# Optimization experiments

Hardware: AMD Instinct MI355X
Metric: run time of the kernel (lower is better)

Reference implementation:

```python
import jax, jax.numpy as jnp
import numpy as np
import math

B, S, IN_DIM, D, L, W = 16, 2048, 32, 512, 6, 3
FF = 4 * D
EPS = 1e-5
MAX_LEN = 5000


def _make_pe(d_model, max_len=MAX_LEN):
    position = np.arange(max_len, dtype=np.float32)[:, None]
    div_term = np.exp(np.arange(0, d_model, 2, dtype=np.float32) * (-math.log(10000.0) / d_model))
    pe = np.zeros((max_len, d_model), np.float32)
    pe[:, 0::2] = np.sin(position * div_term)
    pe[:, 1::2] = np.cos(position * div_term)
    # register_buffer pe: [max_len, 1, d_model] (seq-first layout)
    return jnp.asarray(pe[:, None, :])


def setup_inputs() -> dict:
    key = jax.random.key(0)
    ks = jax.random.split(key, 16)
    s = 0.02
    inp = {
        "src": jax.random.normal(ks[0], (B, S, IN_DIM), jnp.float32),
        "pe": _make_pe(D),
        "enc_w": jax.random.uniform(ks[1], (D, IN_DIM), jnp.float32, -0.1, 0.1),
        "enc_b": jnp.zeros((D,), jnp.float32),
        "l1_w": jax.random.normal(ks[2], (L, FF, D), jnp.float32) * s,
        "l1_b": jnp.zeros((L, FF), jnp.float32),
        "l2_w": jax.random.normal(ks[3], (L, D, FF), jnp.float32) * s,
        "l2_b": jnp.zeros((L, D), jnp.float32),
        "n1_g": jnp.ones((L, D), jnp.float32),
        "n1_b": jnp.zeros((L, D), jnp.float32),
        "n2_g": jnp.ones((L, D), jnp.float32),
        "n2_b": jnp.zeros((L, D), jnp.float32),
        "dec_w": jax.random.uniform(ks[4], (1, D), jnp.float32, -0.1, 0.1),
        "dec_b": jnp.zeros((1,), jnp.float32),
    }
    return inp


def _layernorm(x, g, b):
    mu = jnp.mean(x, axis=-1, keepdims=True)
    var = jnp.var(x, axis=-1, keepdims=True)
    return (x - mu) * jax.lax.rsqrt(var + EPS) * g + b


def _sparse_attention(q, k, v, window):
    # banded local attention: query i attends to keys j with |i-j| <= window
    Bq, Sq, Dq = q.shape
    scale = 1.0 / math.sqrt(Dq)
    offs = jnp.arange(2 * window + 1) - window          # [K]
    idx = jnp.arange(Sq)[:, None] + offs[None, :]        # [S, K]
    valid = (idx >= 0) & (idx < Sq)
    idxc = jnp.clip(idx, 0, Sq - 1)
    kw = k[:, idxc]                                      # [B, S, K, D]
    vw = v[:, idxc]                                      # [B, S, K, D]
    scores = jnp.einsum('bsd,bskd->bsk', q, kw) * scale  # [B, S, K]
    scores = jnp.where(valid[None, :, :], scores, -1e9)
    attn = jax.nn.softmax(scores, axis=-1)
    return jnp.einsum('bsk,bskd->bsd', attn, vw)


def reference(src, pe, enc_w, enc_b, l1_w, l1_b, l2_w, l2_b,
              n1_g, n1_b, n2_g, n2_b, dec_w, dec_b):
    x = src @ enc_w.T + enc_b
    x = x * math.sqrt(D)
    # faithful to original: pe[:x.size(0)] -> [B,1,D] broadcast over seq
    x = x + pe[: x.shape[0]]
    for i in range(L):
        a = _sparse_attention(x, x, x, W)
        x = _layernorm(x + a, n1_g[i], n1_b[i])
        h = jax.nn.relu(x @ l1_w[i].T + l1_b[i])
        f = h @ l2_w[i].T + l2_b[i]
        x = _layernorm(x + f, n2_g[i], n2_b[i])
    out = x[:, -1, :] @ dec_w.T + dec_b  # [B, 1]
    return out
```

## Files before the change

kernel.cpp:

```cpp
#include <hip/hip_runtime.h>
#include <hip/hip_bf16.h>
#include <math.h>

constexpr int Bb  = 16;
constexpr int Ss  = 2048;
constexpr int INd = 32;
constexpr int Dd  = 512;
constexpr int FFf = 2048;
constexpr int Ll  = 6;
constexpr int BS  = Bb * Ss;
constexpr float EPSf = 1e-5f;

typedef __attribute__((ext_vector_type(8))) short short8;
typedef __attribute__((ext_vector_type(4))) float f32x4;

__device__ __forceinline__ ushort f2bf(float f) {
    uint u = __float_as_uint(f);
    uint r = (u + 0x7fffu + ((u >> 16) & 1u)) >> 16;
    return (ushort)r;
}

__global__ __launch_bounds__(256)
void convert_bf16(const float* __restrict__ in, ushort* __restrict__ out, int n4) {
    int i = blockIdx.x * blockDim.x + threadIdx.x;
    int stride = gridDim.x * blockDim.x;
    for (; i < n4; i += stride) {
        float4 v = ((const float4*)in)[i];
        ushort4 o;
        o.x = f2bf(v.x); o.y = f2bf(v.y); o.z = f2bf(v.z); o.w = f2bf(v.w);
        ((ushort4*)out)[i] = o;
    }
}

__global__ __launch_bounds__(256)
void encode_kernel(const float* __restrict__ src, const float* __restrict__ pe,
                   const float* __restrict__ ew, const float* __restrict__ eb,
                   float* __restrict__ y) {
    __shared__ float s_src[8][32];
    const int tid = threadIdx.x;
    const int d0  = 2 * tid;
    float w0[32], w1[32];
    #pragma unroll
    for (int k = 0; k < 32; k += 4) {
        float4 a = *(const float4*)(ew + (size_t)d0 * INd + k);
        float4 b = *(const float4*)(ew + (size_t)(d0 + 1) * INd + k);
        w0[k] = a.x; w0[k+1] = a.y; w0[k+2] = a.z; w0[k+3] = a.w;
        w1[k] = b.x; w1[k+1] = b.y; w1[k+2] = b.z; w1[k+3] = b.w;
    }
    const float e0 = eb[d0], e1 = eb[d0 + 1];
    const float sqrtD = 22.62741699796952f;

    for (int t0 = 0; t0 < BS / 2048; t0 += 8) {
        __syncthreads();
        {
            const int j = tid >> 5, e = tid & 31;
            const int tok = (int)blockIdx.x + (t0 + j) * 2048;
            s_src[j][e] = src[(size_t)tok * INd + e];
        }
        __syncthreads();
        #pragma unroll
        for (int j = 0; j < 8; ++j) {
            const int tok = (int)blockIdx.x + (t0 + j) * 2048;
            const int b   = tok >> 11;
            float a0 = 0.f, a1 = 0.f;
            #pragma unroll
            for (int k = 0; k < 32; ++k) {
                const float sv = s_src[j][k];
                a0 = fmaf(sv, w0[k], a0);
                a1 = fmaf(sv, w1[k], a1);
            }
            const float2 pv = *(const float2*)(pe + (size_t)b * Dd + d0);
            float2 o;
            o.x = (a0 + e0) * sqrtD + pv.x;
            o.y = (a1 + e1) * sqrtD + pv.y;
            *(float2*)(y + (size_t)tok * Dd + d0) = o;
        }
    }
}

__global__ __launch_bounds__(256)
void attn_ln_kernel(const float* __restrict__ x, float* __restrict__ y,
                    ushort* __restrict__ ybf,
                    const float* __restrict__ g, const float* __restrict__ bb) {
    const int wv   = threadIdx.x >> 6;
    const int lane = threadIdx.x & 63;
    const int wid  = blockIdx.x * 4 + wv;
    const int b    = wid >> 11;
    const int s    = wid & (Ss - 1);
    const float* base = x + (size_t)b * Ss * Dd;

    float rows[7][8];
    #pragma unroll
    for (int o = 0; o < 7; ++o) {
        int sp = s + o - 3;
        int sc = sp < 0 ? 0 : (sp > Ss - 1 ? Ss - 1 : sp);
        const float* r = base + (size_t)sc * Dd;
        float4 v0 = *(const float4*)(r + lane * 4);
        float4 v1 = *(const float4*)(r + 256 + lane * 4);
        rows[o][0] = v0.x; rows[o][1] = v0.y; rows[o][2] = v0.z; rows[o][3] = v0.w;
        rows[o][4] = v1.x; rows[o][5] = v1.y; rows[o][6] = v1.z; rows[o][7] = v1.w;
    }

    const float scale = 0.04419417382415922f;
    float score[7];
    #pragma unroll
    for (int o = 0; o < 7; ++o) {
        float p = 0.f;
        #pragma unroll
        for (int j = 0; j < 8; ++j) p = fmaf(rows[3][j], rows[o][j], p);
        #pragma unroll
        for (int m = 1; m < 64; m <<= 1) p += __shfl_xor(p, m, 64);
        int sp = s + o - 3;
        score[o] = (sp >= 0 && sp < Ss) ? p * scale : -1e9f;
    }
    float mx = score[0];
    #pragma unroll
    for (int o = 1; o < 7; ++o) mx = fmaxf(mx, score[o]);
    float w[7], wsum = 0.f;
    #pragma unroll
    for (int o = 0; o < 7; ++o) { w[o] = __expf(score[o] - mx); wsum += w[o]; }
    const float inv = 1.f / wsum;
    #pragma unroll
    for (int o = 0; o < 7; ++o) w[o] *= inv;

    float r2[8];
    #pragma unroll
    for (int j = 0; j < 8; ++j) {
        float acc = rows[3][j];
        #pragma unroll
        for (int o = 0; o < 7; ++o) acc = fmaf(w[o], rows[o][j], acc);
        r2[j] = acc;
    }

    float sm = 0.f, sq = 0.f;
    #pragma unroll
    for (int j = 0; j < 8; ++j) { sm += r2[j]; sq = fmaf(r2[j], r2[j], sq); }
    #pragma unroll
    for (int m = 1; m < 64; m <<= 1) {
        sm += __shfl_xor(sm, m, 64);
        sq += __shfl_xor(sq, m, 64);
    }
    const float mu   = sm * (1.f / Dd);
    const float var  = sq * (1.f / Dd) - mu * mu;
    const float rstd = rsqrtf(var + EPSf);

    const size_t ob = (size_t)wid * Dd;
    float4 g0 = *(const float4*)(g  + lane * 4);
    float4 b0 = *(const float4*)(bb + lane * 4);
    float4 g1 = *(const float4*)(g  + 256 + lane * 4);
    float4 b1 = *(const float4*)(bb + 256 + lane * 4);
    float4 o0, o1;
    o0.x = (r2[0] - mu) * rstd * g0.x + b0.x;
    o0.y = (r2[1] - mu) * rstd * g0.y + b0.y;
    o0.z = (r2[2] - mu) * rstd * g0.z + b0.z;
    o0.w = (r2[3] - mu) * rstd * g0.w + b0.w;
    o1.x = (r2[4] - mu) * rstd * g1.x + b1.x;
    o1.y = (r2[5] - mu) * rstd * g1.y + b1.y;
    o1.z = (r2[6] - mu) * rstd * g1.z + b1.z;
    o1.w = (r2[7] - mu) * rstd * g1.w + b1.w;
    *(float4*)(y + ob + lane * 4)       = o0;
    *(float4*)(y + ob + 256 + lane * 4) = o1;

    ushort4 q0, q1;
    q0.x = f2bf(o0.x); q0.y = f2bf(o0.y); q0.z = f2bf(o0.z); q0.w = f2bf(o0.w);
    q1.x = f2bf(o1.x); q1.y = f2bf(o1.y); q1.z = f2bf(o1.z); q1.w = f2bf(o1.w);
    *(ushort4*)(ybf + ob + lane * 4)       = q0;
    *(ushort4*)(ybf + ob + 256 + lane * 4) = q1;
}

__global__ __launch_bounds__(256)
void add_ln_kernel(const float* __restrict__ xres, float* __restrict__ f,
                   const float* __restrict__ g, const float* __restrict__ bb) {
    const int wv   = threadIdx.x >> 6;
    const int lane = threadIdx.x & 63;
    const int wid  = blockIdx.x * 4 + wv;
    const size_t ob = (size_t)wid * Dd;

    float4 a0 = *(const float4*)(xres + ob + lane * 4);
    float4 f0 = *(const float4*)(f    + ob + lane * 4);
    float4 a1 = *(const float4*)(xres + ob + 256 + lane * 4);
    float4 f1 = *(const float4*)(f    + ob + 256 + lane * 4);
    float r2[8];
    r2[0] = a0.x + f0.x; r2[1] = a0.y + f0.y; r2[2] = a0.z + f0.z; r2[3] = a0.w + f0.w;
    r2[4] = a1.x + f1.x; r2[5] = a1.y + f1.y; r2[6] = a1.z + f1.z; r2[7] = a1.w + f1.w;

    float sm = 0.f, sq = 0.f;
    #pragma unroll
    for (int j = 0; j < 8; ++j) { sm += r2[j]; sq = fmaf(r2[j], r2[j], sq); }
    #pragma unroll
    for (int m = 1; m < 64; m <<= 1) {
        sm += __shfl_xor(sm, m, 64);
        sq += __shfl_xor(sq, m, 64);
    }
    const float mu   = sm * (1.f / Dd);
    const float var  = sq * (1.f / Dd) - mu * mu;
    const float rstd = rsqrtf(var + EPSf);

    float4 g0 = *(const float4*)(g  + lane * 4);
    float4 b0 = *(const float4*)(bb + lane * 4);
    float4 g1 = *(const float4*)(g  + 256 + lane * 4);
    float4 b1 = *(const float4*)(bb + 256 + lane * 4);
    float4 o0, o1;
    o0.x = (r2[0] - mu) * rstd * g0.x + b0.x;
    o0.y = (r2[1] - mu) * rstd * g0.y + b0.y;
    o0.z = (r2[2] - mu) * rstd * g0.z + b0.z;
    o0.w = (r2[3] - mu) * rstd * g0.w + b0.w;
    o1.x = (r2[4] - mu) * rstd * g1.x + b1.x;
    o1.y = (r2[5] - mu) * rstd * g1.y + b1.y;
    o1.z = (r2[6] - mu) * rstd * g1.z + b1.z;
    o1.w = (r2[7] - mu) * rstd * g1.w + b1.w;
    *(float4*)(f + ob + lane * 4)       = o0;
    *(float4*)(f + ob + 256 + lane * 4) = o1;
}

template<int RELU, int BF16OUT>
__global__ __launch_bounds__(256)
void gemm_bf16(const ushort* __restrict__ A, const ushort* __restrict__ B,
               const float* __restrict__ bias, void* __restrict__ Cout,
               int M, int N, int K) {
    __shared__ ushort As[128 * 32];
    __shared__ ushort Bs[128 * 32];
    const int tid  = threadIdx.x;
    const int wid  = tid >> 6;
    const int lane = tid & 63;
    const int wr   = wid >> 1;
    const int wc   = wid & 1;

    const int nwg  = (int)(gridDim.x * gridDim.y);
    const int orig = (int)(blockIdx.y * gridDim.x + blockIdx.x);
    const int q    = nwg >> 3, r = nwg & 7;
    const int xcd  = orig & 7, seq = orig >> 3;
    const int swz  = (xcd < r ? xcd * (q + 1) : r * (q + 1) + (xcd - r) * q) + seq;
    const int bxT  = swz % (int)gridDim.x;
    const int byT  = swz / (int)gridDim.x;
    const size_t bm = (size_t)byT * 128;
    const size_t bn = (size_t)bxT * 128;

    const ushort* gA0 = A + (bm + wid * 32 + (lane >> 2)) * (size_t)K + (lane & 3) * 8;
    const ushort* gA1 = gA0 + (size_t)16 * K;
    const ushort* gB0 = B + (bn + wid * 32 + (lane >> 2)) * (size_t)K + (lane & 3) * 8;
    const ushort* gB1 = gB0 + (size_t)16 * K;
    ushort* lA0 = &As[wid * 1024];
    ushort* lA1 = lA0 + 512;
    ushort* lB0 = &Bs[wid * 1024];
    ushort* lB1 = lB0 + 512;

    const ushort* aPtr = &As[(wr * 64 + (lane & 15)) * 32 + (lane >> 4) * 8];
    const ushort* bPtr = &Bs[(wc * 64 + (lane & 15)) * 32 + (lane >> 4) * 8];

    f32x4 acc[4][4];
    #pragma unroll
    for (int i = 0; i < 4; ++i)
        #pragma unroll
        for (int j = 0; j < 4; ++j) acc[i][j] = (f32x4){0.f, 0.f, 0.f, 0.f};

    #define GLDS(gp, lp) __builtin_amdgcn_global_load_lds( \
        (const __attribute__((address_space(1))) void*)(gp), \
        (__attribute__((address_space(3))) void*)(lp), 16, 0, 0)

    for (int k0 = 0; k0 < K; k0 += 32) {
        GLDS(gA0 + k0, lA0);
        GLDS(gA1 + k0, lA1);
        GLDS(gB0 + k0, lB0);
        GLDS(gB1 + k0, lB1);
        __syncthreads();
        short8 af[4], bf_[4];
        #pragma unroll
        for (int mt = 0; mt < 4; ++mt) af[mt]  = *(const short8*)(aPtr + mt * 512);
        #pragma unroll
        for (int nt = 0; nt < 4; ++nt) bf_[nt] = *(const short8*)(bPtr + nt * 512);
        #pragma unroll
        for (int mt = 0; mt < 4; ++mt)
            #pragma unroll
            for (int nt = 0; nt < 4; ++nt)
                acc[mt][nt] = __builtin_amdgcn_mfma_f32_16x16x32_bf16(
                    af[mt], bf_[nt], acc[mt][nt], 0, 0, 0);
        __syncthreads();
    }
    #undef GLDS

    float* Cf  = (float*)Cout;
    ushort* Cb = (ushort*)Cout;
    #pragma unroll
    for (int nt = 0; nt < 4; ++nt) {
        const int cn = (int)bn + wc * 64 + nt * 16 + (lane & 15);
        const float bv = bias[cn];
        #pragma unroll
        for (int mt = 0; mt < 4; ++mt) {
            const size_t rowb = bm + wr * 64 + mt * 16 + (lane >> 4) * 4;
            #pragma unroll
            for (int rr = 0; rr < 4; ++rr) {
                float v = acc[mt][nt][rr] + bv;
                if (RELU) v = fmaxf(v, 0.f);
                if (BF16OUT) Cb[(rowb + rr) * (size_t)N + cn] = f2bf(v);
                else         Cf[(rowb + rr) * (size_t)N + cn] = v;
            }
        }
    }
}

__global__ __launch_bounds__(64)
void decode_kernel(const float* __restrict__ x, const float* __restrict__ dw,
                   const float* __restrict__ db, float* __restrict__ out) {
    const int b = blockIdx.x;
    const int lane = threadIdx.x;
    const float* r = x + ((size_t)b * Ss + (Ss - 1)) * Dd;
    float acc = 0.f;
    #pragma unroll
    for (int j = 0; j < 8; ++j) acc = fmaf(r[j*64 + lane], dw[j*64 + lane], acc);
    #pragma unroll
    for (int m = 1; m < 64; m <<= 1) acc += __shfl_xor(acc, m, 64);
    if (lane == 0) out[b] = acc + db[0];
}

extern "C" void kernel_launch(void* const* d_in, const int* in_sizes, int n_in,
                              void* d_out, int out_size, void* d_ws, size_t ws_size,
                              hipStream_t stream) {
    const float* src   = (const float*)d_in[0];
    const float* pe    = (const float*)d_in[1];
    const float* enc_w = (const float*)d_in[2];
    const float* enc_b = (const float*)d_in[3];
    const float* l1_w  = (const float*)d_in[4];
    const float* l1_b  = (const float*)d_in[5];
    const float* l2_w  = (const float*)d_in[6];
    const float* l2_b  = (const float*)d_in[7];
    const float* n1_g  = (const float*)d_in[8];
    const float* n1_b  = (const float*)d_in[9];
    const float* n2_g  = (const float*)d_in[10];
    const float* n2_b  = (const float*)d_in[11];
    const float* dec_w = (const float*)d_in[12];
    const float* dec_b = (const float*)d_in[13];
    float* out = (float*)d_out;

    const size_t NTOK = (size_t)BS * Dd;
    float*  xA   = (float*)d_ws;
    float*  xB   = xA + NTOK;
    ushort* xBbf = (ushort*)(xB + NTOK);
    ushort* w1bf = xBbf + NTOK;
    ushort* w2bf = w1bf + (size_t)Ll * FFf * Dd;
    ushort* hbf  = w2bf + (size_t)Ll * FFf * Dd;

    const size_t fixedBytes = (size_t)((char*)hbf - (char*)d_ws);
    size_t hBytes = ws_size > fixedBytes ? ws_size - fixedBytes : 0;
    int    chunkM = (int)(hBytes / ((size_t)FFf * sizeof(ushort)));
    if (chunkM > BS) chunkM = BS;
    chunkM &= ~127;
    if (chunkM < 128) chunkM = 128;

    const int wn4 = Ll * FFf * Dd / 4;
    convert_bf16<<<1024, 256, 0, stream>>>(l1_w, w1bf, wn4);
    convert_bf16<<<1024, 256, 0, stream>>>(l2_w, w2bf, wn4);

    encode_kernel<<<2048, 256, 0, stream>>>(src, pe, enc_w, enc_b, xA);

    for (int i = 0; i < Ll; ++i) {
        attn_ln_kernel<<<BS / 4, 256, 0, stream>>>(
            xA, xB, xBbf, n1_g + i * Dd, n1_b + i * Dd);
        for (int m0 = 0; m0 < BS; m0 += chunkM) {
            int mh = (BS - m0) < chunkM ? (BS - m0) : chunkM;
            gemm_bf16<1, 1><<<dim3(FFf / 128, mh / 128), 256, 0, stream>>>(
                xBbf + (size_t)m0 * Dd, w1bf + (size_t)i * FFf * Dd,
                l1_b + i * FFf, hbf, mh, FFf, Dd);
            gemm_bf16<0, 0><<<dim3(Dd / 128, mh / 128), 256, 0, stream>>>(
                hbf, w2bf + (size_t)i * Dd * FFf, l2_b + i * Dd,
                xA + (size_t)m0 * Dd, mh, Dd, FFf);
        }
        add_ln_kernel<<<BS / 4, 256, 0, stream>>>(
            xB, xA, n2_g + i * Dd, n2_b + i * Dd);
    }

    decode_kernel<<<Bb, 64, 0, stream>>>(xA, dec_w, dec_b, out);
}
```

Before: 2.010 ms.

## Fuse post-FFN add+LayerNorm with next layer's banded attention and LayerNorm

Replaces the separate add_ln and attn_ln kernels between layers with one kernel that recomputes residual+LayerNorm for each row in the 7-token window, then runs the banded attention and the first LayerNorm of the next layer. This removes one full-tensor write and reread of the fp32 activations per layer, at the cost of recomputing LayerNorm for every neighbouring row (7x redundant reductions). It also adds a block-index swizzle to the attention kernels and double-buffers the residual tensor.

```diff
diff --git a/kernel.cpp b/kernel.cpp
--- a/kernel.cpp
+++ b/kernel.cpp
@@ -78,13 +78,17 @@
     }
 }
 
+__device__ __forceinline__ int swz_block(int ob, int nb) {
+    return (ob & 7) * (nb >> 3) + (ob >> 3);
+}
+
 __global__ __launch_bounds__(256)
 void attn_ln_kernel(const float* __restrict__ x, float* __restrict__ y,
                     ushort* __restrict__ ybf,
                     const float* __restrict__ g, const float* __restrict__ bb) {
     const int wv   = threadIdx.x >> 6;
     const int lane = threadIdx.x & 63;
-    const int wid  = blockIdx.x * 4 + wv;
+    const int wid  = swz_block((int)blockIdx.x, (int)gridDim.x) * 4 + wv;
     const int b    = wid >> 11;
     const int s    = wid & (Ss - 1);
     const float* base = x + (size_t)b * Ss * Dd;
@@ -158,6 +162,126 @@
     o1.y = (r2[5] - mu) * rstd * g1.y + b1.y;
     o1.z = (r2[6] - mu) * rstd * g1.z + b1.z;
     o1.w = (r2[7] - mu) * rstd * g1.w + b1.w;
+    *(float4*)(y + ob + lane * 4)       = o0;
+    *(float4*)(y + ob + 256 + lane * 4) = o1;
+
+    ushort4 q0, q1;
+    q0.x = f2bf(o0.x); q0.y = f2bf(o0.y); q0.z = f2bf(o0.z); q0.w = f2bf(o0.w);
+    q1.x = f2bf(o1.x); q1.y = f2bf(o1.y); q1.z = f2bf(o1.z); q1.w = f2bf(o1.w);
+    *(ushort4*)(ybf + ob + lane * 4)       = q0;
+    *(ushort4*)(ybf + ob + 256 + lane * 4) = q1;
+}
+
+__global__ __launch_bounds__(256)
+void fused_tail_attn_kernel(const float* __restrict__ xb, const float* __restrict__ ff,
+                            const float* __restrict__ g2, const float* __restrict__ b2,
+                            const float* __restrict__ g1, const float* __restrict__ b1,
+                            float* __restrict__ y, ushort* __restrict__ ybf) {
+    const int wv   = threadIdx.x >> 6;
+    const int lane = threadIdx.x & 63;
+    const int wid  = swz_block((int)blockIdx.x, (int)gridDim.x) * 4 + wv;
+    const int b    = wid >> 11;
+    const int s    = wid & (Ss - 1);
+    const size_t roff = (size_t)b * Ss * Dd;
+
+    float4 G2a = *(const float4*)(g2 + lane * 4);
+    float4 G2b = *(const float4*)(g2 + 256 + lane * 4);
+    float4 B2a = *(const float4*)(b2 + lane * 4);
+    float4 B2b = *(const float4*)(b2 + 256 + lane * 4);
+
+    float rows[7][8];
+    #pragma unroll
+    for (int o = 0; o < 7; ++o) {
+        int sp = s + o - 3;
+        int sc = sp < 0 ? 0 : (sp > Ss - 1 ? Ss - 1 : sp);
+        const float* xr = xb + roff + (size_t)sc * Dd;
+        const float* fr = ff + roff + (size_t)sc * Dd;
+        float4 x0 = *(const float4*)(xr + lane * 4);
+        float4 f0 = *(const float4*)(fr + lane * 4);
+        float4 x1 = *(const float4*)(xr + 256 + lane * 4);
+        float4 f1 = *(const float4*)(fr + 256 + lane * 4);
+        float r2[8];
+        r2[0] = x0.x + f0.x; r2[1] = x0.y + f0.y; r2[2] = x0.z + f0.z; r2[3] = x0.w + f0.w;
+        r2[4] = x1.x + f1.x; r2[5] = x1.y + f1.y; r2[6] = x1.z + f1.z; r2[7] = x1.w + f1.w;
+
+        float sm = 0.f, sq = 0.f;
+        #pragma unroll
+        for (int j = 0; j < 8; ++j) { sm += r2[j]; sq = fmaf(r2[j], r2[j], sq); }
+        #pragma unroll
+        for (int m = 1; m < 64; m <<= 1) {
+            sm += __shfl_xor(sm, m, 64);
+            sq += __shfl_xor(sq, m, 64);
+        }
+        const float mu   = sm * (1.f / Dd);
+        const float var  = sq * (1.f / Dd) - mu * mu;
+        const float rstd = rsqrtf(var + EPSf);
+        rows[o][0] = (r2[0] - mu) * rstd * G2a.x + B2a.x;
+        rows[o][1] = (r2[1] - mu) * rstd * G2a.y + B2a.y;
+        rows[o][2] = (r2[2] - mu) * rstd * G2a.z + B2a.z;
+        rows[o][3] = (r2[3] - mu) * rstd * G2a.w + B2a.w;
+        rows[o][4] = (r2[4] - mu) * rstd * G2b.x + B2b.x;
+        rows[o][5] = (r2[5] - mu) * rstd * G2b.y + B2b.y;
+        rows[o][6] = (r2[6] - mu) * rstd * G2b.z + B2b.z;
+        rows[o][7] = (r2[7] - mu) * rstd * G2b.w + B2b.w;
+    }
+
+    const float scale = 0.04419417382415922f;
+    float score[7];
+    #pragma unroll
+    for (int o = 0; o < 7; ++o) {
+        float p = 0.f;
+        #pragma unroll
+        for (int j = 0; j < 8; ++j) p = fmaf(rows[3][j], rows[o][j], p);
+        #pragma unroll
+        for (int m = 1; m < 64; m <<= 1) p += __shfl_xor(p, m, 64);
+        int sp = s + o - 3;
+        score[o] = (sp >= 0 && sp < Ss) ? p * scale : -1e9f;
+    }
+    float mx = score[0];
+    #pragma unroll
+    for (int o = 1; o < 7; ++o) mx = fmaxf(mx, score[o]);
+    float w[7], wsum = 0.f;
+    #pragma unroll
+    for (int o = 0; o < 7; ++o) { w[o] = __expf(score[o] - mx); wsum += w[o]; }
+    const float inv = 1.f / wsum;
+    #pragma unroll
+    for (int o = 0; o < 7; ++o) w[o] *= inv;
+
+    float r2[8];
+    #pragma unroll
+    for (int j = 0; j < 8; ++j) {
+        float acc = rows[3][j];
+        #pragma unroll
+        for (int o = 0; o < 7; ++o) acc = fmaf(w[o], rows[o][j], acc);
+        r2[j] = acc;
+    }
+
+    float sm = 0.f, sq = 0.f;
+    #pragma unroll
+    for (int j = 0; j < 8; ++j) { sm += r2[j]; sq = fmaf(r2[j], r2[j], sq); }
+    #pragma unroll
+    for (int m = 1; m < 64; m <<= 1) {
+        sm += __shfl_xor(sm, m, 64);
+        sq += __shfl_xor(sq, m, 64);
+    }
+    const float mu   = sm * (1.f / Dd);
+    const float var  = sq * (1.f / Dd) - mu * mu;
+    const float rstd = rsqrtf(var + EPSf);
+
+    const size_t ob = (size_t)wid * Dd;
+    float4 g0 = *(const float4*)(g1 + lane * 4);
+    float4 b0 = *(const float4*)(b1 + lane * 4);
+    float4 g1v = *(const float4*)(g1 + 256 + lane * 4);
+    float4 b1v = *(const float4*)(b1 + 256 + lane * 4);
+    float4 o0, o1;
+    o0.x = (r2[0] - mu) * rstd * g0.x + b0.x;
+    o0.y = (r2[1] - mu) * rstd * g0.y + b0.y;
+    o0.z = (r2[2] - mu) * rstd * g0.z + b0.z;
+    o0.w = (r2[3] - mu) * rstd * g0.w + b0.w;
+    o1.x = (r2[4] - mu) * rstd * g1v.x + b1v.x;
+    o1.y = (r2[5] - mu) * rstd * g1v.y + b1v.y;
+    o1.z = (r2[6] - mu) * rstd * g1v.z + b1v.z;
+    o1.w = (r2[7] - mu) * rstd * g1v.w + b1v.w;
     *(float4*)(y + ob + lane * 4)       = o0;
     *(float4*)(y + ob + 256 + lane * 4) = o1;
 
@@ -333,9 +457,10 @@
     float* out = (float*)d_out;
 
     const size_t NTOK = (size_t)BS * Dd;
-    float*  xA   = (float*)d_ws;
-    float*  xB   = xA + NTOK;
-    ushort* xBbf = (ushort*)(xB + NTOK);
+    float*  fbuf = (float*)d_ws;
+    float*  xBa  = fbuf + NTOK;
+    float*  xBb  = xBa + NTOK;
+    ushort* xBbf = (ushort*)(xBb + NTOK);
     ushort* w1bf = xBbf + NTOK;
     ushort* w2bf = w1bf + (size_t)Ll * FFf * Dd;
     ushort* hbf  = w2bf + (size_t)Ll * FFf * Dd;
@@ -351,11 +476,14 @@
     convert_bf16<<<1024, 256, 0, stream>>>(l1_w, w1bf, wn4);
     convert_bf16<<<1024, 256, 0, stream>>>(l2_w, w2bf, wn4);
 
-    encode_kernel<<<2048, 256, 0, stream>>>(src, pe, enc_w, enc_b, xA);
-
+    encode_kernel<<<2048, 256, 0, stream>>>(src, pe, enc_w, enc_b, fbuf);
+
+    attn_ln_kernel<<<BS / 4, 256, 0, stream>>>(
+        fbuf, xBa, xBbf, n1_g, n1_b);
+
+    float* curXB = xBa;
+    float* nxtXB = xBb;
     for (int i = 0; i < Ll; ++i) {
-        attn_ln_kernel<<<BS / 4, 256, 0, stream>>>(
-            xA, xB, xBbf, n1_g + i * Dd, n1_b + i * Dd);
         for (int m0 = 0; m0 < BS; m0 += chunkM) {
             int mh = (BS - m0) < chunkM ? (BS - m0) : chunkM;
             gemm_bf16<1, 1><<<dim3(FFf / 128, mh / 128), 256, 0, stream>>>(
@@ -363,11 +491,20 @@
                 l1_b + i * FFf, hbf, mh, FFf, Dd);
             gemm_bf16<0, 0><<<dim3(Dd / 128, mh / 128), 256, 0, stream>>>(
                 hbf, w2bf + (size_t)i * Dd * FFf, l2_b + i * Dd,
-                xA + (size_t)m0 * Dd, mh, Dd, FFf);
+                fbuf + (size_t)m0 * Dd, mh, Dd, FFf);
         }
-        add_ln_kernel<<<BS / 4, 256, 0, stream>>>(
-            xB, xA, n2_g + i * Dd, n2_b + i * Dd);
-    }
-
-    decode_kernel<<<Bb, 64, 0, stream>>>(xA, dec_w, dec_b, out);
-}
+        if (i < Ll - 1) {
+            fused_tail_attn_kernel<<<BS / 4, 256, 0, stream>>>(
+                curXB, fbuf,
+                n2_g + i * Dd, n2_b + i * Dd,
+                n1_g + (i + 1) * Dd, n1_b + (i + 1) * Dd,
+                nxtXB, xBbf);
+            float* t = curXB; curXB = nxtXB; nxtXB = t;
+        } else {
+            add_ln_kernel<<<BS / 4, 256, 0, stream>>>(
+                curXB, fbuf, n2_g + i * Dd, n2_b + i * Dd);
+        }
+    }
+
+    decode_kernel<<<Bb, 64, 0, stream>>>(fbuf, dec_w, dec_b, out);
+}
```

New measurement: 6.086 ms. 203% more time.
